# Optimization experiments

Hardware: AMD Instinct MI355X
Metric: run time of the kernel (lower is better)

## Reference

```python
import jax, jax.numpy as jnp
import numpy as np

N, E, H = 25000, 100000, 32          # nodes, edges, node/clique hidden dim
NC, A, EC = 8000, 50000, 24000       # cliques, node2clique assignments, clique edges
EEMB, CEE, L = 8, 8, 2               # edge emb dims, n layers


def segment_mean(vals, ids, num):
    s = jax.ops.segment_sum(vals, ids, num_segments=num)
    cnt = jax.ops.segment_sum(jnp.ones(ids.shape[0], vals.dtype), ids, num_segments=num)
    return s / jnp.maximum(cnt, 1.0)[:, None]


def setup_inputs() -> dict:
    key = jax.random.key(0)
    ks = jax.random.split(key, 24)
    s = 0.1  # param scale
    inp = {
        "node_features": jax.random.normal(ks[0], (N, H), jnp.float32),
        "edge_index": jax.random.randint(ks[1], (2, E), 0, N),
        "edge_features": jax.random.normal(ks[2], (E, EEMB), jnp.float32),
        "clique_features": jax.random.normal(ks[3], (NC, H), jnp.float32),
        "node2clique_index": jnp.stack([
            jax.random.randint(ks[4], (A,), 0, N),
            jax.random.randint(ks[5], (A,), 0, NC)]),
        "clique_edge_index": jax.random.randint(ks[6], (2, EC), 0, NC),
        "clique_edge_features": jax.random.normal(ks[7], (EC, CEE), jnp.float32),
        # node NNConv params (stacked over L layers)
        "nn1_w": jax.random.normal(ks[8], (L, EEMB, H)) * s,
        "nn1_b": jnp.zeros((L, H)),
        "nn2_w": jax.random.normal(ks[9], (L, H, H * H)) * s,
        "nn2_b": jnp.zeros((L, H * H)),
        "root_w": jax.random.normal(ks[10], (L, H, H)) * s,
        "root_b": jnp.zeros((L, H)),
        # Node2Clique linear
        "n2c_w": jax.random.normal(ks[11], (L, H, H)) * s,
        "n2c_b": jnp.zeros((L, H)),
        # clique NNConv params
        "cnn1_w": jax.random.normal(ks[12], (L, CEE, H)) * s,
        "cnn1_b": jnp.zeros((L, H)),
        "cnn2_w": jax.random.normal(ks[13], (L, H, H * H)) * s,
        "cnn2_b": jnp.zeros((L, H * H)),
        "croot_w": jax.random.normal(ks[14], (L, H, H)) * s,
        "croot_b": jnp.zeros((L, H)),
        # Clique2Node linear
        "c2n_w": jax.random.normal(ks[15], (L, H, H)) * s,
        "c2n_b": jnp.zeros((L, H)),
    }
    return inp


def nnconv(x, src, dst, edge_attr, w1, b1, w2, b2, rw, rb, n_out_nodes):
    # per-edge weight matrices from the edge MLP: [E, in, out]
    h = jax.nn.relu(edge_attr @ w1 + b1)
    We = (h @ w2 + b2).reshape(edge_attr.shape[0], x.shape[1], -1)
    msg = jnp.einsum('ei,eio->eo', x[src], We)           # message from source
    agg = segment_mean(msg, dst, n_out_nodes)            # mean aggregation at target
    return agg + x @ rw + rb                             # root weight + bias


def reference(node_features, edge_index, edge_features, clique_features,
              node2clique_index, clique_edge_index, clique_edge_features,
              nn1_w, nn1_b, nn2_w, nn2_b, root_w, root_b, n2c_w, n2c_b,
              cnn1_w, cnn1_b, cnn2_w, cnn2_b, croot_w, croot_b, c2n_w, c2n_b):
    x, c = node_features, clique_features
    src, dst = edge_index[0], edge_index[1]
    nid, cid = node2clique_index[0], node2clique_index[1]
    csrc, cdst = clique_edge_index[0], clique_edge_index[1]
    for l in range(L):
        # node-level edge-conditioned conv
        x = jax.nn.relu(nnconv(x, src, dst, edge_features,
                               nn1_w[l], nn1_b[l], nn2_w[l], nn2_b[l],
                               root_w[l], root_b[l], N))
        # Node2Clique: project node feats, scatter-mean into cliques
        m = x @ n2c_w[l] + n2c_b[l]
        c = c + segment_mean(m[nid], cid, NC)
        # clique-level edge-conditioned conv
        c = jax.nn.relu(nnconv(c, csrc, cdst, clique_edge_features,
                               cnn1_w[l], cnn1_b[l], cnn2_w[l], cnn2_b[l],
                               croot_w[l], croot_b[l], NC))
        # Clique2Node: project clique feats, scatter-mean back onto nodes
        m = c @ c2n_w[l] + c2n_b[l]
        x = x + segment_mean(m[cid], nid, N)
    return (x, c)
```

## Files before the change

### kernel.cpp

```cpp
#include <hip/hip_runtime.h>
#include <hip/hip_bf16.h>

typedef unsigned int u32;
typedef unsigned short u16;

#define DEVINL __device__ __forceinline__

constexpr int Nn  = 25000;
constexpr int Ee  = 100000;
constexpr int NCc = 8000;
constexpr int Aa  = 50000;
constexpr int ECc = 24000;
constexpr int TCOLS = 1088;
constexpr int WPSZ  = TCOLS*32;
constexpr int TT_ROW = 561;
constexpr int NB_N = (Nn + 255)/256;
constexpr int NB_C = (NCc + 255)/256;
constexpr int NSEGB = 3*(NB_N + NB_C);
constexpr int PB_EN = (Ee + 255)/256;
constexpr int PB_EC = (ECc + 255)/256;
constexpr int PB_AS = (2*Aa + 255)/256;
constexpr int PB_WP = (4*WPSZ + 255)/256;

typedef float f32x4 __attribute__((ext_vector_type(4)));
typedef _Float16 h16x2 __attribute__((ext_vector_type(2)));
typedef _Float16 h16x8 __attribute__((ext_vector_type(8)));

DEVINL float b2f(u16 u){ union{u32 i;float f;}v; v.i = ((u32)u)<<16; return v.f; }
DEVINL float bfl(u32 u){ union{u32 i;float f;}v; v.i = u<<16; return v.f; }
DEVINL float bfh(u32 u){ union{u32 i;float f;}v; v.i = u & 0xffff0000u; return v.f; }
DEVINL u16 f2b(float f){ union{float f;u32 i;}v; v.f=f; u32 i=v.i;
  return (u16)((i + 0x7fffu + ((i>>16)&1u)) >> 16); }
DEVINL u16 f2h(float x){ union{ _Float16 h; u16 u; } v; v.h = (_Float16)x; return v.u; }
DEVINL u32 pkh2(float a, float b){
  union{ _Float16 h[2]; u32 u; } v;
  v.h[0] = (_Float16)a; v.h[1] = (_Float16)b; return v.u;
}
DEVINL float ldw(const void* p, long i, int f){
  return f ? ((const float*)p)[i] : b2f(((const u16*)p)[i]);
}
DEVINL float dot2f(u32 a, u32 b, float c){
  union U{u32 u; h16x2 h;};
  U ua; ua.u = a; U ub; ub.u = b;
#if __has_builtin(__builtin_amdgcn_fdot2)
  return __builtin_amdgcn_fdot2(ua.h, ub.h, c, false);
#else
  return c + (float)ua.h[0]*(float)ub.h[0] + (float)ua.h[1]*(float)ub.h[1];
#endif
}

__global__ __launch_bounds__(256) void k_detect_count(const u16* __restrict__ p, int n,
                        u32* __restrict__ maxbits, int* __restrict__ zcnt,
                        int* __restrict__ done, int* __restrict__ flag,
                        const int* __restrict__ ei, const int* __restrict__ cei,
                        const int* __restrict__ n2c,
                        int* __restrict__ deg_nd, int* __restrict__ deg_ce,
                        int* __restrict__ deg_n2c, int* __restrict__ deg_c2n,
                        int* __restrict__ cnt_sn, int* __restrict__ cnt_sc){
  int i0 = blockIdx.x*256 + threadIdx.x;
  { int t = i0;
    if (t < Ee)                             atomicAdd(&deg_nd[ei[Ee + t]], 1);
    else if ((t -= Ee) < ECc)               atomicAdd(&deg_ce[cei[ECc + t]], 1);
    else if ((t -= ECc) < Aa)               atomicAdd(&deg_n2c[n2c[Aa + t]], 1);
    else if ((t -= Aa) < Aa)                atomicAdd(&deg_c2n[n2c[t]], 1);
    else if ((t -= Aa) < Ee)                atomicAdd(&cnt_sn[ei[t]], 1);
    else if ((t -= Ee) < ECc)               atomicAdd(&cnt_sc[cei[t]], 1);
  }
  if (blockIdx.x >= 256) return;
  float lm = 0.f; int lz = 0;
  for (int i = i0; i < n; i += 256*256){
    u16 v = p[i];
    if (v == 0) lz++;
    lm = fmaxf(lm, fabsf(b2f(v)));
  }
  #pragma unroll
  for (int off = 32; off; off >>= 1){
    lm = fmaxf(lm, __shfl_down(lm, off));
    lz += __shfl_down(lz, off);
  }
  __shared__ float smax[4]; __shared__ int szc[4];
  if ((threadIdx.x & 63) == 0){
    smax[threadIdx.x >> 6] = lm;
    szc[threadIdx.x >> 6] = lz;
  }
  __syncthreads();
  if (threadIdx.x == 0){
    float m = fmaxf(fmaxf(smax[0], smax[1]), fmaxf(smax[2], smax[3]));
    int z = szc[0] + szc[1] + szc[2] + szc[3];
    atomicMax(maxbits, __float_as_uint(m));
    atomicAdd(zcnt, z);
    __threadfence();
    if (atomicAdd(done, 1) == 255){
      float mm = __uint_as_float(*maxbits);
      *flag = (mm > 1e6f || *zcnt > n/4) ? 1 : 0;
    }
  }
}

DEVINL void segof(int bid, int& seg, int& rb){
  seg = 0; rb = bid;
  while (true){
    int nb = (seg & 1) ? NB_C : NB_N;
    if (rb < nb) break;
    rb -= nb; seg++;
  }
}

__global__ __launch_bounds__(256) void k_scan1(
    const int* __restrict__ c0, const int* __restrict__ c1,
    const int* __restrict__ c2, const int* __restrict__ c3,
    const int* __restrict__ c4, const int* __restrict__ c5,
    int* __restrict__ o0, int* __restrict__ o1, int* __restrict__ o2,
    int* __restrict__ o3, int* __restrict__ o4, int* __restrict__ o5){
  __shared__ int s[256];
  __shared__ int red[256];
  int seg, rb; segof(blockIdx.x, seg, rb);
  const int* cnt; int* offs;
  switch (seg){
    case 0: cnt=c0; offs=o0; break;
    case 1: cnt=c1; offs=o1; break;
    case 2: cnt=c2; offs=o2; break;
    case 3: cnt=c3; offs=o3; break;
    case 4: cnt=c4; offs=o4; break;
    default: cnt=c5; offs=o5; break;
  }
  int M = (seg & 1) ? NCc : Nn;
  int t = threadIdx.x;
  int part = 0;
  for (int j = t; j < rb*256; j += 256) part += cnt[j];
  red[t] = part; __syncthreads();
  #pragma unroll
  for (int d = 128; d; d >>= 1){
    if (t < d) red[t] += red[t + d];
    __syncthreads();
  }
  int prefix = red[0];
  int i = rb*256 + t;
  int v = (i < M) ? cnt[i] : 0;
  s[t] = v; __syncthreads();
  for (int d = 1; d < 256; d <<= 1){
    int tv = (t >= d) ? s[t-d] : 0;
    __syncthreads();
    s[t] += tv;
    __syncthreads();
  }
  if (i < M) offs[i] = prefix + s[t] - v;
}

__global__ __launch_bounds__(256) void k_place_pack(
    const int* __restrict__ ei, const int* __restrict__ cei, const int* __restrict__ n2c,
    const void* __restrict__ ef, const void* __restrict__ cef,
    const void* __restrict__ nn1w, const void* __restrict__ nn1b,
    const void* __restrict__ cnn1w, const void* __restrict__ cnn1b,
    const void* __restrict__ nn2w, const void* __restrict__ nn2b, const void* __restrict__ rootw,
    const void* __restrict__ cnn2w, const void* __restrict__ cnn2b, const void* __restrict__ crootw,
    const int* __restrict__ offs_n, const int* __restrict__ offs_c,
    const int* __restrict__ offs_an, const int* __restrict__ offs_ac,
    const int* __restrict__ doffs_n, const int* __restrict__ doffs_c,
    int* __restrict__ cur_n, int* __restrict__ cur_c,
    int* __restrict__ cur_an, int* __restrict__ cur_ac,
    int* __restrict__ cur_dn, int* __restrict__ cur_dc,
    int2* __restrict__ sdp_n, int2* __restrict__ sdp_c,
    u32* __restrict__ hp_n, u32* __restrict__ hp_c,
    int* __restrict__ an2c, int* __restrict__ ac2n,
    const int* __restrict__ flag, u16* __restrict__ Wp4){
  int b = blockIdx.x, tid = threadIdx.x;
  int f = *flag;
  if (b < PB_EN + PB_EC){
    __shared__ float w1s[2][256], b1s[2][32];
    int isC = (b >= PB_EN);
    int e = (isC ? b - PB_EN : b)*256 + tid;
    int E = isC ? ECc : Ee;
    const void* W1 = isC ? cnn1w : nn1w;
    const void* B1 = isC ? cnn1b : nn1b;
    w1s[0][tid] = ldw(W1, tid, f);
    w1s[1][tid] = ldw(W1, 256 + tid, f);
    if (tid < 32){ b1s[0][tid] = ldw(B1, tid, f); b1s[1][tid] = ldw(B1, 32 + tid, f); }
    __syncthreads();
    if (e < E){
      const int* EI = isC ? cei : ei;
      int s = EI[e], d = EI[E + e];
      int* cur = isC ? cur_c : cur_n;
      const int* offs = isC ? offs_c : offs_n;
      int p = offs[s] + atomicAdd(&cur[s], 1);
      const int* dofs = isC ? doffs_c : doffs_n;
      int* curd = isC ? cur_dc : cur_dn;
      int dsl = dofs[d] + atomicAdd(&curd[d], 1);
      (isC ? sdp_c : sdp_n)[p] = make_int2(s, dsl);
      const void* EF = isC ? cef : ef;
      float ev[8];
      #pragma unroll
      for (int j = 0; j < 8; j++) ev[j] = ldw(EF, (long)e*8 + j, f);
      u32* hp = isC ? hp_c : hp_n;
      #pragma unroll
      for (int l = 0; l < 2; l++){
        u32* hq = hp + (size_t)l*E*16 + (size_t)p*16;
        #pragma unroll
        for (int kk = 0; kk < 16; kk++){
          float a0 = b1s[l][2*kk], a1 = b1s[l][2*kk+1];
          #pragma unroll
          for (int j = 0; j < 8; j++){
            a0 += ev[j]*w1s[l][j*32 + 2*kk];
            a1 += ev[j]*w1s[l][j*32 + 2*kk + 1];
          }
          hq[kk] = pkh2(fmaxf(a0, 0.f), fmaxf(a1, 0.f));
        }
      }
    }
  } else if (b < PB_EN + PB_EC + PB_AS){
    int i = (b - PB_EN - PB_EC)*256 + tid;
    if (i < Aa){
      int c = n2c[Aa + i];
      an2c[offs_ac[c] + atomicAdd(&cur_ac[c], 1)] = n2c[i];
    } else if ((i -= Aa) < Aa){
      int nd = n2c[i];
      ac2n[offs_an[nd] + atomicAdd(&cur_an[nd], 1)] = n2c[Aa + i];
    }
  } else {
    int i = (b - PB_EN - PB_EC - PB_AS)*256 + tid;
    if (i >= 4*WPSZ) return;
    int set = i / WPSZ, j = i - set*WPSZ;
    int l = set >> 1, isC = set & 1;
    const void* W2 = isC ? cnn2w : nn2w;
    const void* B2 = isC ? cnn2b : nn2b;
    const void* RW = isC ? crootw : rootw;
    int col = j >> 5, ii = j & 31;
    float v;
    if (col < 1024)      v = ldw(W2, (long)l*32768 + ((col>>5)<<10) + (ii<<5) + (col&31), f);
    else if (col < 1056) v = ldw(B2, (long)l*1024 + (ii<<5) + (col-1024), f);
    else                 v = ldw(RW, (long)l*1024 + (ii<<5) + (col-1056), f);
    Wp4[i] = f2h(v);
  }
}

__global__ __launch_bounds__(512) void k_conv_fused(const void* __restrict__ base, int braw,
                           const float* __restrict__ adm, const int* __restrict__ sidx,
                           const int* __restrict__ soffs, const int* __restrict__ sdeg, int M,
                           const int2* __restrict__ sdp, const u32* __restrict__ hp,
                           const int* __restrict__ offs, int E_,
                           const u16* __restrict__ Wp,
                           const void* __restrict__ rb, long rboff,
                           const int* __restrict__ flag,
                           float* __restrict__ feat_root, u32* __restrict__ msgp){
  __shared__ __align__(16) u32 Tt[16*TT_ROW];
  __shared__ __align__(16) u32 hws[8][64];
  int tid = threadIdx.x;
  int w = tid >> 6, lane = tid & 63;
  int quad = lane >> 4, lm = lane & 15;
  int n0 = blockIdx.x * 16;
  int f = *flag;
  int n = n0 + lm;
  int nc = n < M ? n : M-1;
  long bidx = (long)nc*32 + quad*8;
  float fv[8];
  if (braw && f == 0){
    uint4 q = *(const uint4*)((const u16*)base + bidx);
    fv[0]=bfl(q.x); fv[1]=bfh(q.x); fv[2]=bfl(q.y); fv[3]=bfh(q.y);
    fv[4]=bfl(q.z); fv[5]=bfh(q.z); fv[6]=bfl(q.w); fv[7]=bfh(q.w);
  } else {
    const float4* bp = (const float4*)((const float*)base + bidx);
    float4 q0 = bp[0], q1 = bp[1];
    fv[0]=q0.x; fv[1]=q0.y; fv[2]=q0.z; fv[3]=q0.w;
    fv[4]=q1.x; fv[5]=q1.y; fv[6]=q1.z; fv[7]=q1.w;
  }
  if (adm){
    int slo = soffs[nc], scnt = sdeg[nc];
    float ac[8] = {0,0,0,0,0,0,0,0};
    for (int k = 0; k < scnt; k++){
      const float4* mp = (const float4*)(adm + (size_t)sidx[slo + k]*32 + quad*8);
      float4 a0 = mp[0], a1 = mp[1];
      ac[0]+=a0.x; ac[1]+=a0.y; ac[2]+=a0.z; ac[3]+=a0.w;
      ac[4]+=a1.x; ac[5]+=a1.y; ac[6]+=a1.z; ac[7]+=a1.w;
    }
    float inv = 1.f/(float)(scnt > 1 ? scnt : 1);
    #pragma unroll
    for (int j = 0; j < 8; j++) fv[j] += ac[j]*inv;
  }
  union { h16x8 v; u32 u[4]; } bf;
  #pragma unroll
  for (int j = 0; j < 4; j++) bf.u[j] = pkh2(fv[2*j], fv[2*j+1]);

  #define AFR(ct) (*(const h16x8*)(Wp + (size_t)((ct)*16 + lm)*32 + quad*8))
  f32x4 z4 = {0.f, 0.f, 0.f, 0.f};
  #pragma unroll
  for (int g = 0; g < 2; g++){
    int q = w + 8*g;
    f32x4 c0 = __builtin_amdgcn_mfma_f32_16x16x32_f16(AFR(4*q+0), bf.v, z4, 0, 0, 0);
    f32x4 c1 = __builtin_amdgcn_mfma_f32_16x16x32_f16(AFR(4*q+1), bf.v, z4, 0, 0, 0);
    f32x4 c2 = __builtin_amdgcn_mfma_f32_16x16x32_f16(AFR(4*q+2), bf.v, z4, 0, 0, 0);
    f32x4 c3 = __builtin_amdgcn_mfma_f32_16x16x32_f16(AFR(4*q+3), bf.v, z4, 0, 0, 0);
    int rbase = lm*TT_ROW;
    int ob = quad*4;
    #pragma unroll
    for (int i = 0; i < 4; i++){
      Tt[rbase + (ob+i)*17 + q]      = pkh2(c0[i], c2[i]);
      Tt[rbase + (16+ob+i)*17 + q]   = pkh2(c1[i], c3[i]);
    }
  }
  if (w < 4){
    int ct = 64 + w;
    f32x4 c = __builtin_amdgcn_mfma_f32_16x16x32_f16(AFR(ct), bf.v, z4, 0, 0, 0);
    if (ct < 66){
      int p0 = (ct-64)*8 + quad*2;
      Tt[lm*TT_ROW + 544 + p0]     = pkh2(c[0], c[1]);
      Tt[lm*TT_ROW + 544 + p0 + 1] = pkh2(c[2], c[3]);
    } else if (n < M){
      int o = (ct-66)*16 + quad*4;
      float4 v = make_float4(c[0] + ldw(rb, rboff+o,   f),
                             c[1] + ldw(rb, rboff+o+1, f),
                             c[2] + ldw(rb, rboff+o+2, f),
                             c[3] + ldw(rb, rboff+o+3, f));
      *(float4*)&feat_root[(size_t)n*32 + o] = v;
    }
  }
  __syncthreads();

  int lo = offs[n0];
  int hi = (n0 + 16 < M) ? offs[n0 + 16] : E_;
  int eg = quad, kk = lm;
  int pos = lo + w*4;
  u32 hp0 = 0, hp1 = 0; int sd0 = 0, sd1 = 0;
  { int idx = pos*16 + lane;      if (idx < hi*16) hp0 = hp[idx];
    idx = (pos+32)*16 + lane;     if (idx < hi*16) hp1 = hp[idx]; }
  if (lane < 8){
    int idx = pos*2 + lane;       if (idx < hi*2) sd0 = ((const int*)sdp)[idx];
    idx = (pos+32)*2 + lane;      if (idx < hi*2) sd1 = ((const int*)sdp)[idx];
  }
  for (; pos < hi; pos += 32){
    int np = pos + 64;
    u32 hp2 = 0; int sd2 = 0;
    { int idx = np*16 + lane; if (idx < hi*16) hp2 = hp[idx]; }
    if (lane < 8){ int idx = np*2 + lane; if (idx < hi*2) sd2 = ((const int*)sdp)[idx]; }
    hws[w][lane] = hp0;
    int sn = __shfl(sd0, 2*eg);
    int ds = __shfl(sd0, 2*eg + 1);
    bool valid = (pos + eg < hi);
    int sr = sn - n0; sr = sr < 0 ? 0 : (sr > 15 ? 15 : sr);
    const u32* Tr = Tt + sr*TT_ROW;
    const u32* T0 = Tr + 34*kk;
    const uint4* Hp4 = (const uint4*)&hws[w][eg*16];
    union{u32 u; h16x2 h;} b2u; b2u.u = Tr[544 + kk];
    float m0 = (float)b2u.h[0], m1 = (float)b2u.h[1];
    #pragma unroll
    for (int g = 0; g < 4; g++){
      uint4 hv4 = Hp4[g];
      m0 = dot2f(hv4.x, T0[4*g+0], m0);  m1 = dot2f(hv4.x, T0[17+4*g+0], m1);
      m0 = dot2f(hv4.y, T0[4*g+1], m0);  m1 = dot2f(hv4.y, T0[17+4*g+1], m1);
      m0 = dot2f(hv4.z, T0[4*g+2], m0);  m1 = dot2f(hv4.z, T0[17+4*g+2], m1);
      m0 = dot2f(hv4.w, T0[4*g+3], m0);  m1 = dot2f(hv4.w, T0[17+4*g+3], m1);
    }
    if (valid){
      msgp[(size_t)ds*16 + kk] = pkh2(m0, m1);
    }
    hp0 = hp1; sd0 = sd1; hp1 = hp2; sd1 = sd2;
  }
  #undef AFR
}

__global__ __launch_bounds__(256) void k_update_lin(const u32* __restrict__ msgp,
                           const int* __restrict__ doffs, const int* __restrict__ deg,
                           const float* __restrict__ feat_root, int M,
                           const void* __restrict__ w, long woff,
                           const void* __restrict__ b, long boff,
                           const int* __restrict__ flag,
                           float* __restrict__ feat, float* __restrict__ mout,
                           void* __restrict__ outp){
  __shared__ float wsm[1024], bs[32], rows[8][33];
  int tid = threadIdx.x;
  int f = *flag;
  for (int idx = tid; idx < 1024; idx += 256) wsm[idx] = ldw(w, woff + idx, f);
  if (tid < 32) bs[tid] = ldw(b, boff + tid, f);
  int nl = tid >> 5, o = tid & 31;
  int n = blockIdx.x*8 + nl;
  long i = (long)n*32 + o;
  if (n < M){
    int lo = doffs[n], dg = deg[n];
    float a = 0.f;
    for (int k = 0; k < dg; k++){
      union{u32 u; h16x2 h;} c;
      c.u = msgp[(size_t)(lo + k)*16 + (o >> 1)];
      a += (float)c.h[o & 1];
    }
    float d = (float)(dg > 1 ? dg : 1);
    float v = fmaxf(a/d + feat_root[i], 0.f);
    rows[nl][o] = v;
    feat[i] = v;
    if (outp){
      long oi = (long)Nn*32 + i;
      if (f) ((float*)outp)[oi] = v;
      else   ((u16*)outp)[oi]   = f2b(v);
    }
  }
  __syncthreads();
  if (n >= M) return;
  float acc = bs[o];
  #pragma unroll
  for (int j = 0; j < 32; j++) acc += rows[nl][j]*wsm[j*32+o];
  mout[i] = acc;
}

__global__ __launch_bounds__(256) void k_store(const float* __restrict__ x,
                      const float* __restrict__ mC, const int* __restrict__ sidx,
                      const int* __restrict__ soffs, const int* __restrict__ sdeg,
                      void* __restrict__ out, const int* __restrict__ flag){
  int i = blockIdx.x*256 + threadIdx.x;
  if (i >= Nn*32) return;
  int n = i >> 5, o = i & 31;
  int lo = soffs[n], dg = sdeg[n];
  float a = 0.f;
  for (int k = 0; k < dg; k++) a += mC[(size_t)sidx[lo + k]*32 + o];
  float v = x[i] + a/(float)(dg > 1 ? dg : 1);
  if (*flag) ((float*)out)[i] = v;
  else       ((u16*)out)[i]   = f2b(v);
}

extern "C" void kernel_launch(void* const* d_in, const int* in_sizes, int n_in,
                              void* d_out, int out_size, void* d_ws, size_t ws_size,
                              hipStream_t stream){
  const int* ei  = (const int*)d_in[1];
  const int* n2c = (const int*)d_in[4];
  const int* cei = (const int*)d_in[5];
  const void *efr = d_in[2], *cefr = d_in[6];
  const void *nn1w = d_in[7], *nn1b = d_in[8], *nn2w = d_in[9], *nn2b = d_in[10],
             *rootw = d_in[11], *rootb = d_in[12], *n2cw = d_in[13], *n2cb = d_in[14],
             *cnn1w = d_in[15], *cnn1b = d_in[16], *cnn2w = d_in[17], *cnn2b = d_in[18],
             *crootw = d_in[19], *crootb = d_in[20], *c2nw = d_in[21], *c2nb = d_in[22];

  char* ws = (char*)d_ws;
  size_t off = 0;
  auto alloc = [&](size_t bytes){ void* p = ws + off; off += (bytes + 255) & ~(size_t)255; return p; };

  size_t zstart = off;
  int* deg_nd  = (int*)alloc((size_t)Nn*4);
  int* deg_ce  = (int*)alloc((size_t)NCc*4);
  int* deg_n2c = (int*)alloc((size_t)NCc*4);
  int* deg_c2n = (int*)alloc((size_t)Nn*4);
  int* cnt_sn  = (int*)alloc((size_t)Nn*4);
  int* cnt_sc  = (int*)alloc((size_t)NCc*4);
  int* cur_n   = (int*)alloc((size_t)Nn*4);
  int* cur_c   = (int*)alloc((size_t)NCc*4);
  int* cur_an  = (int*)alloc((size_t)Nn*4);
  int* cur_ac  = (int*)alloc((size_t)NCc*4);
  int* cur_dn  = (int*)alloc((size_t)Nn*4);
  int* cur_dc  = (int*)alloc((size_t)NCc*4);
  u32* maxbits = (u32*)alloc(256);
  int* zcnt = (int*)((char*)maxbits + 4);
  int* flag = (int*)((char*)maxbits + 8);
  int* done = (int*)((char*)maxbits + 12);
  size_t zbytes = off - zstart;

  float* xB  = (float*)alloc((size_t)Nn*32*4);
  float* xC  = (float*)alloc((size_t)Nn*32*4);
  float* cC0 = (float*)alloc((size_t)NCc*32*4);
  float* cC1 = (float*)alloc((size_t)NCc*32*4);
  float* frn = (float*)alloc((size_t)Nn*32*4);
  float* frc = (float*)alloc((size_t)NCc*32*4);
  u32* msgN = (u32*)alloc((size_t)Ee*16*4);
  u32* msgC = (u32*)alloc((size_t)ECc*16*4);
  float* mN  = (float*)alloc((size_t)Nn*32*4);
  float* mC  = (float*)alloc((size_t)NCc*32*4);
  int* offs_n  = (int*)alloc((size_t)Nn*4);
  int* offs_c  = (int*)alloc((size_t)NCc*4);
  int* offs_an = (int*)alloc((size_t)Nn*4);
  int* offs_ac = (int*)alloc((size_t)NCc*4);
  int* doffs_n = (int*)alloc((size_t)Nn*4);
  int* doffs_c = (int*)alloc((size_t)NCc*4);
  int* an2c = (int*)alloc((size_t)Aa*4);
  int* ac2n = (int*)alloc((size_t)Aa*4);
  int2* sdp_n = (int2*)alloc((size_t)Ee*8);
  int2* sdp_c = (int2*)alloc((size_t)ECc*8);
  u16* Wp4 = (u16*)alloc((size_t)4*WPSZ*2);
  u32* hp_n = (u32*)alloc((size_t)2*Ee*16*4);
  u32* hp_c = (u32*)alloc((size_t)2*ECc*16*4);

  auto nb = [](int n){ return (n + 255)/256; };

  hipMemsetAsync(ws + zstart, 0, zbytes, stream);
  k_detect_count<<<nb(2*Ee + 2*ECc + 2*Aa),256,0,stream>>>((const u16*)d_in[0], Nn*32,
      maxbits, zcnt, done, flag, ei, cei, n2c,
      deg_nd, deg_ce, deg_n2c, deg_c2n, cnt_sn, cnt_sc);
  k_scan1<<<NSEGB,256,0,stream>>>(cnt_sn, cnt_sc, deg_c2n, deg_n2c, deg_nd, deg_ce,
      offs_n, offs_c, offs_an, offs_ac, doffs_n, doffs_c);
  k_place_pack<<<PB_EN+PB_EC+PB_AS+PB_WP,256,0,stream>>>(ei, cei, n2c, efr, cefr,
      nn1w, nn1b, cnn1w, cnn1b, nn2w, nn2b, rootw, cnn2w, cnn2b, crootw,
      offs_n, offs_c, offs_an, offs_ac, doffs_n, doffs_c,
      cur_n, cur_c, cur_an, cur_ac, cur_dn, cur_dc,
      sdp_n, sdp_c, hp_n, hp_c, an2c, ac2n, flag, Wp4);

  int Gn = (Nn + 15)/16, Gc = (NCc + 15)/16;

  k_conv_fused<<<Gn,512,0,stream>>>(d_in[0], 1, nullptr, nullptr, nullptr, nullptr, Nn,
      sdp_n, hp_n, offs_n, Ee, Wp4 + 0*WPSZ, rootb, 0, flag, frn, msgN);
  k_update_lin<<<(Nn+7)/8,256,0,stream>>>(msgN, doffs_n, deg_nd, frn, Nn,
      n2cw, 0, n2cb, 0, flag, xB, mN, nullptr);
  k_conv_fused<<<Gc,512,0,stream>>>(d_in[3], 1, mN, an2c, offs_ac, deg_n2c, NCc,
      sdp_c, hp_c, offs_c, ECc, Wp4 + 1*WPSZ, crootb, 0, flag, frc, msgC);
  k_update_lin<<<(NCc+7)/8,256,0,stream>>>(msgC, doffs_c, deg_ce, frc, NCc,
      c2nw, 0, c2nb, 0, flag, cC0, mC, nullptr);
  k_conv_fused<<<Gn,512,0,stream>>>(xB, 0, mC, ac2n, offs_an, deg_c2n, Nn,
      sdp_n, hp_n + (size_t)Ee*16, offs_n, Ee, Wp4 + 2*WPSZ, rootb, 32, flag, frn, msgN);
  k_update_lin<<<(Nn+7)/8,256,0,stream>>>(msgN, doffs_n, deg_nd, frn, Nn,
      n2cw, 1024, n2cb, 32, flag, xC, mN, nullptr);
  k_conv_fused<<<Gc,512,0,stream>>>(cC0, 0, mN, an2c, offs_ac, deg_n2c, NCc,
      sdp_c, hp_c + (size_t)ECc*16, offs_c, ECc, Wp4 + 3*WPSZ, crootb, 32, flag, frc, msgC);
  k_update_lin<<<(NCc+7)/8,256,0,stream>>>(msgC, doffs_c, deg_ce, frc, NCc,
      c2nw, 1024, c2nb, 32, flag, cC1, mC, d_out);
  k_store<<<nb(Nn*32),256,0,stream>>>(xC, mC, ac2n, offs_an, deg_c2n, d_out, flag);
}
```

Measured before the change: 291.8 us.

## Interleave per-layer edge hidden vectors and vectorize input detection scan

The per-edge hidden activations for both layers are now stored interleaved (32 words per edge) instead of as two separate layer planes. Each edge's place-pack write becomes one contiguous 128-byte span, and the conv kernel reads a 64-byte half with a stride of 32 words. The bf16 detection scan in the count kernel now loads uint4 vectors and handles 8 values per load instead of single u16 loads. In exchange, conv reads become strided half-lines rather than fully contiguous, and the vector scan assumes n is a multiple of 8.

```diff
diff --git a/kernel.cpp b/kernel.cpp
--- a/kernel.cpp
+++ b/kernel.cpp
@@ -68,10 +68,19 @@
   }
   if (blockIdx.x >= 256) return;
   float lm = 0.f; int lz = 0;
-  for (int i = i0; i < n; i += 256*256){
-    u16 v = p[i];
-    if (v == 0) lz++;
-    lm = fmaxf(lm, fabsf(b2f(v)));
+  const uint4* pv = (const uint4*)p;
+  int nv = n >> 3;
+  for (int i = i0; i < nv; i += 256*256){
+    uint4 q = pv[i];
+    u32 wv[4] = {q.x, q.y, q.z, q.w};
+    #pragma unroll
+    for (int j = 0; j < 4; j++){
+      u32 x = wv[j];
+      if ((x & 0xffffu) == 0) lz++;
+      if ((x >> 16) == 0) lz++;
+      lm = fmaxf(lm, fabsf(bfl(x)));
+      lm = fmaxf(lm, fabsf(bfh(x)));
+    }
   }
   #pragma unroll
   for (int off = 32; off; off >>= 1){
@@ -191,10 +200,9 @@
       float ev[8];
       #pragma unroll
       for (int j = 0; j < 8; j++) ev[j] = ldw(EF, (long)e*8 + j, f);
-      u32* hp = isC ? hp_c : hp_n;
+      u32* hq = (isC ? hp_c : hp_n) + (size_t)p*32;
       #pragma unroll
       for (int l = 0; l < 2; l++){
-        u32* hq = hp + (size_t)l*E*16 + (size_t)p*16;
         #pragma unroll
         for (int kk = 0; kk < 16; kk++){
           float a0 = b1s[l][2*kk], a1 = b1s[l][2*kk+1];
@@ -203,7 +211,7 @@
             a0 += ev[j]*w1s[l][j*32 + 2*kk];
             a1 += ev[j]*w1s[l][j*32 + 2*kk + 1];
           }
-          hq[kk] = pkh2(fmaxf(a0, 0.f), fmaxf(a1, 0.f));
+          hq[l*16 + kk] = pkh2(fmaxf(a0, 0.f), fmaxf(a1, 0.f));
         }
       }
     }
@@ -318,10 +326,12 @@
   int lo = offs[n0];
   int hi = (n0 + 16 < M) ? offs[n0 + 16] : E_;
   int eg = quad, kk = lm;
+  int le = lane >> 4, wk = lane & 15;
   int pos = lo + w*4;
   u32 hp0 = 0, hp1 = 0; int sd0 = 0, sd1 = 0;
-  { int idx = pos*16 + lane;      if (idx < hi*16) hp0 = hp[idx];
-    idx = (pos+32)*16 + lane;     if (idx < hi*16) hp1 = hp[idx]; }
+  { int ep = pos + le;
+    if (ep < hi)      hp0 = hp[(size_t)ep*32 + wk];
+    if (ep + 32 < hi) hp1 = hp[(size_t)(ep + 32)*32 + wk]; }
   if (lane < 8){
     int idx = pos*2 + lane;       if (idx < hi*2) sd0 = ((const int*)sdp)[idx];
     idx = (pos+32)*2 + lane;      if (idx < hi*2) sd1 = ((const int*)sdp)[idx];
@@ -329,7 +339,7 @@
   for (; pos < hi; pos += 32){
     int np = pos + 64;
     u32 hp2 = 0; int sd2 = 0;
-    { int idx = np*16 + lane; if (idx < hi*16) hp2 = hp[idx]; }
+    { int ep = np + le; if (ep < hi) hp2 = hp[(size_t)ep*32 + wk]; }
     if (lane < 8){ int idx = np*2 + lane; if (idx < hi*2) sd2 = ((const int*)sdp)[idx]; }
     hws[w][lane] = hp0;
     int sn = __shfl(sd0, 2*eg);
@@ -470,8 +480,8 @@
   int2* sdp_n = (int2*)alloc((size_t)Ee*8);
   int2* sdp_c = (int2*)alloc((size_t)ECc*8);
   u16* Wp4 = (u16*)alloc((size_t)4*WPSZ*2);
-  u32* hp_n = (u32*)alloc((size_t)2*Ee*16*4);
-  u32* hp_c = (u32*)alloc((size_t)2*ECc*16*4);
+  u32* hp_n = (u32*)alloc((size_t)Ee*32*4);
+  u32* hp_c = (u32*)alloc((size_t)ECc*32*4);
 
   auto nb = [](int n){ return (n + 255)/256; };
 
@@ -498,11 +508,11 @@
   k_update_lin<<<(NCc+7)/8,256,0,stream>>>(msgC, doffs_c, deg_ce, frc, NCc,
       c2nw, 0, c2nb, 0, flag, cC0, mC, nullptr);
   k_conv_fused<<<Gn,512,0,stream>>>(xB, 0, mC, ac2n, offs_an, deg_c2n, Nn,
-      sdp_n, hp_n + (size_t)Ee*16, offs_n, Ee, Wp4 + 2*WPSZ, rootb, 32, flag, frn, msgN);
+      sdp_n, hp_n + 16, offs_n, Ee, Wp4 + 2*WPSZ, rootb, 32, flag, frn, msgN);
   k_update_lin<<<(Nn+7)/8,256,0,stream>>>(msgN, doffs_n, deg_nd, frn, Nn,
       n2cw, 1024, n2cb, 32, flag, xC, mN, nullptr);
   k_conv_fused<<<Gc,512,0,stream>>>(cC0, 0, mN, an2c, offs_ac, deg_n2c, NCc,
-      sdp_c, hp_c + (size_t)ECc*16, offs_c, ECc, Wp4 + 3*WPSZ, crootb, 32, flag, frc, msgC);
+      sdp_c, hp_c + 16, offs_c, ECc, Wp4 + 3*WPSZ, crootb, 32, flag, frc, msgC);
   k_update_lin<<<(NCc+7)/8,256,0,stream>>>(msgC, doffs_c, deg_ce, frc, NCc,
       c2nw, 1024, c2nb, 32, flag, cC1, mC, d_out);
   k_store<<<nb(Nn*32),256,0,stream>>>(xC, mC, ac2n, offs_an, deg_c2n, d_out, flag);
```

Measured after the change: 291.6 us. No clear change (-0.1%).
